# Performance work log

Hardware: AMD Instinct MI355X
Metric: run time of the kernel (lower is better)

The kernel has to match this reference:

```python
import jax, jax.numpy as jnp
import numpy as np

D_MODEL, N_LAYERS, D_INNER, D_STATE, D_CONV, DT_RANK, NUM_CLASSES = 256, 4, 512, 16, 4, 16, 10
B, L = 8, 1024


def setup_inputs() -> dict:
    key = jax.random.key(0)
    ks = jax.random.split(key, 16)
    s = 0.02
    inp = {}
    inp['x'] = jax.random.normal(ks[0], (B, L, 1), jnp.float32)
    inp['input_w'] = jax.random.normal(ks[1], (D_MODEL, 1), jnp.float32) * s
    inp['input_b'] = jnp.zeros((D_MODEL,), jnp.float32)
    inp['ln_w'] = jnp.ones((N_LAYERS, D_MODEL), jnp.float32)
    inp['ln_b'] = jnp.zeros((N_LAYERS, D_MODEL), jnp.float32)
    inp['in_proj_w'] = jax.random.normal(ks[2], (N_LAYERS, 2 * D_INNER, D_MODEL), jnp.float32) * s
    inp['in_proj_b'] = jnp.zeros((N_LAYERS, 2 * D_INNER), jnp.float32)
    inp['conv_w'] = jax.random.normal(ks[3], (N_LAYERS, D_INNER, 1, D_CONV), jnp.float32) * 0.2
    inp['conv_b'] = jnp.zeros((N_LAYERS, D_INNER), jnp.float32)
    inp['x_proj_w'] = jax.random.normal(ks[4], (N_LAYERS, DT_RANK + 2 * D_STATE, D_INNER), jnp.float32) * s
    inp['dt_proj_w'] = jax.random.normal(ks[5], (N_LAYERS, D_INNER, DT_RANK), jnp.float32) * s
    inp['dt_proj_b'] = jax.random.normal(ks[6], (N_LAYERS, D_INNER), jnp.float32) * 0.1 - 4.0  # small softplus(dt)
    # canonical S4D-real init: A = [1..d_state] repeated over d_inner
    A = jnp.tile(jnp.arange(1, D_STATE + 1, dtype=jnp.float32)[None, :], (D_INNER, 1))
    inp['A_log'] = jnp.tile(jnp.log(A)[None], (N_LAYERS, 1, 1))
    inp['D'] = jnp.ones((N_LAYERS, D_INNER), jnp.float32)
    inp['out_proj_w'] = jax.random.normal(ks[7], (N_LAYERS, D_MODEL, D_INNER), jnp.float32) * s
    inp['out_proj_b'] = jnp.zeros((N_LAYERS, D_MODEL), jnp.float32)
    inp['norm_w'] = jnp.ones((D_MODEL,), jnp.float32)
    inp['norm_b'] = jnp.zeros((D_MODEL,), jnp.float32)
    inp['cls_w'] = jax.random.normal(ks[8], (NUM_CLASSES, D_MODEL), jnp.float32) * s
    inp['cls_b'] = jnp.zeros((NUM_CLASSES,), jnp.float32)
    return inp


def _layernorm(x, w, b, eps=1e-5):
    mu = jnp.mean(x, axis=-1, keepdims=True)
    var = jnp.mean(jnp.square(x - mu), axis=-1, keepdims=True)
    return (x - mu) * jax.lax.rsqrt(var + eps) * w + b


def _causal_depthwise_conv(u, w, b):
    # u: (B, L, D_inner), w: (D_inner, 1, K), causal padding K-1
    out = jax.lax.conv_general_dilated(
        u.transpose(0, 2, 1), w, window_strides=(1,), padding=[(D_CONV - 1, 0)],
        feature_group_count=D_INNER, dimension_numbers=('NCH', 'OIH', 'NCH'))
    return out.transpose(0, 2, 1) + b


def _selective_scan(u, delta, A, Bm, Cm, Dp):
    # u, delta: (B,L,Din); Bm, Cm: (B,L,N); A: (Din,N); Dp: (Din,)
    def step(h, inp):
        d_t, B_t, C_t, u_t = inp                       # (B,Din),(B,N),(B,N),(B,Din)
        dA = jnp.exp(d_t[:, :, None] * A)              # (B,Din,N)
        dBu = d_t[:, :, None] * B_t[:, None, :] * u_t[:, :, None]
        h = dA * h + dBu
        y = jnp.einsum('bdn,bn->bd', h, C_t)
        return h, y
    h0 = jnp.zeros((u.shape[0], D_INNER, D_STATE), u.dtype)
    xs = (delta.transpose(1, 0, 2), Bm.transpose(1, 0, 2), Cm.transpose(1, 0, 2), u.transpose(1, 0, 2))
    _, ys = jax.lax.scan(step, h0, xs)                 # ys: (L,B,Din)
    return ys.transpose(1, 0, 2) + u * Dp


def _mamba_layer(x, ln_w, ln_b, ipw, ipb, cw, cb, xpw, dtw, dtb, A_log, Dp, opw, opb):
    h = _layernorm(x, ln_w, ln_b)
    xz = jnp.einsum('bld,ed->ble', h, ipw) + ipb       # (B,L,2*Din)
    u, res = jnp.split(xz, 2, axis=-1)
    u = jax.nn.silu(_causal_depthwise_conv(u, cw, cb))
    x_dbl = jnp.einsum('bld,ed->ble', u, xpw)          # (B,L,dt_rank+2N)
    dt, Bm, Cm = jnp.split(x_dbl, [DT_RANK, DT_RANK + D_STATE], axis=-1)
    delta = jax.nn.softplus(jnp.einsum('blr,dr->bld', dt, dtw) + dtb)
    A = -jnp.exp(A_log)
    y = _selective_scan(u, delta, A, Bm, Cm, Dp)
    y = y * jax.nn.silu(res)
    return x + jnp.einsum('ble,de->bld', y, opw) + opb


def reference(x, input_w, input_b, ln_w, ln_b, in_proj_w, in_proj_b, conv_w, conv_b,
              x_proj_w, dt_proj_w, dt_proj_b, A_log, D, out_proj_w, out_proj_b,
              norm_w, norm_b, cls_w, cls_b):
    h = jnp.einsum('blc,dc->bld', x, input_w) + input_b   # (B,L,D_MODEL)
    for i in range(N_LAYERS):
        h = _mamba_layer(h, ln_w[i], ln_b[i], in_proj_w[i], in_proj_b[i], conv_w[i], conv_b[i],
                         x_proj_w[i], dt_proj_w[i], dt_proj_b[i], A_log[i], D[i],
                         out_proj_w[i], out_proj_b[i])
    h = _layernorm(h, norm_w, norm_b)
    pooled = jnp.mean(h, axis=1)                          # (B, D_MODEL)
    return jnp.einsum('bd,cd->bc', pooled, cls_w) + cls_b
```

## Files before the change

kernel.cpp:

```cpp
#include <hip/hip_runtime.h>
#include <hip/hip_bf16.h>
#include <math.h>

#define DM 256
#define NL 4
#define DI 512
#define DS 16
#define DC 4
#define DR 16
#define NC 10
#define NB 8
#define LL 1024
#define MR (NB*LL)
#define NCHUNK 64
#define CLEN 16

typedef __attribute__((ext_vector_type(4))) float f32x4;
typedef __attribute__((ext_vector_type(8))) short short8;

__device__ __forceinline__ float silu_f(float x) {
    return x * (1.0f / (1.0f + __expf(-x)));
}
__device__ __forceinline__ float bf2f(ushort v) {
    union { unsigned u; float f; } c; c.u = ((unsigned)v) << 16; return c.f;
}
__device__ __forceinline__ ushort f2bf(float f) {
    union { float f; unsigned u; } c; c.f = f;
    unsigned lsb = (c.u >> 16) & 1;
    return (ushort)((c.u + 0x7fffu + lsb) >> 16);
}
__device__ __forceinline__ void g2lds16(const void* g, void* l) {
    __builtin_amdgcn_global_load_lds((const __attribute__((address_space(1))) void*)g,
                                     (__attribute__((address_space(3))) void*)l, 16, 0, 0);
}

#define IPW_N (NL*2*DI*DM)
#define XPW_N (NL*64*DI)
#define OPW_N (NL*DM*DI)
__global__ __launch_bounds__(256) void convert_weights_kernel(
        const float* __restrict__ ipw, const float* __restrict__ xpw,
        const float* __restrict__ opw,
        ushort* __restrict__ ipw_b, ushort* __restrict__ xpw_b, ushort* __restrict__ opw_b) {
    int t = blockIdx.x * 256 + threadIdx.x;
    if (t < IPW_N) { ipw_b[t] = f2bf(ipw[t]); return; }
    t -= IPW_N;
    if (t < XPW_N) {
        int l = t >> 15, r = (t >> 9) & 63, k = t & 511;
        xpw_b[t] = (r < 48) ? f2bf(xpw[((size_t)l * 48 + r) * DI + k]) : (ushort)0;
        return;
    }
    t -= XPW_N;
    if (t < OPW_N) opw_b[t] = f2bf(opw[t]);
}

__global__ void input_proj_kernel(const float* __restrict__ x, const float* __restrict__ w,
                                  const float* __restrict__ b, float* __restrict__ h) {
    int t = blockIdx.x * 256 + threadIdx.x;
    if (t >= MR * DM) return;
    int d = t & (DM - 1);
    int m = t >> 8;
    h[t] = x[m] * w[d] + b[d];
}

__global__ __launch_bounds__(256) void layernorm_bf16_kernel(const float* __restrict__ in,
        const float* __restrict__ w, const float* __restrict__ b, ushort* __restrict__ out) {
    int row = blockIdx.x, t = threadIdx.x;
    float v = in[row * DM + t];
    float s = v, q = v * v;
#pragma unroll
    for (int o = 32; o >= 1; o >>= 1) { s += __shfl_xor(s, o); q += __shfl_xor(q, o); }
    __shared__ float red[8];
    int wid = t >> 6;
    if ((t & 63) == 0) { red[wid] = s; red[4 + wid] = q; }
    __syncthreads();
    s = red[0] + red[1] + red[2] + red[3];
    q = red[4] + red[5] + red[6] + red[7];
    float mu = s * (1.0f / DM);
    float var = q * (1.0f / DM) - mu * mu;
    float rs = rsqrtf(var + 1e-5f);
    out[row * DM + t] = f2bf((v - mu) * rs * w[t] + b[t]);
}

template<int BM, int BN, int WM, int WN, int MODE>
__global__ __launch_bounds__(256) void mfma_gemm_kernel(
        const ushort* __restrict__ A, int lda,
        const ushort* __restrict__ W,
        const float* __restrict__ bias,
        ushort* __restrict__ Cb, float* __restrict__ Cf, int ldc, int K) {
    constexpr int FM = BM / WM / 16;
    constexpr int FN = BN / WN / 16;
    __shared__ __align__(16) char smem[(BM + BN) * 128];
    const int tid = threadIdx.x;
    const int l = tid & 63, w = tid >> 6;
    const int wr = w / WN, wc = w % WN;
    const int bm = blockIdx.x * BM, bn = blockIdx.y * BN;
    const int ldw = K;

    f32x4 acc[FM][FN] = {};

    for (int k0 = 0; k0 < K; k0 += 64) {
#pragma unroll
        for (int i = 0; i < (BM * 128 / 16) / 256; i++) {
            int lin = (i * 256 + tid) * 16;
            int q = lin ^ (((lin >> 7) & 7) << 4);
            g2lds16(A + (size_t)(bm + (q >> 7)) * lda + k0 + ((q & 127) >> 1), smem + lin);
        }
#pragma unroll
        for (int i = 0; i < (BN * 128 / 16) / 256; i++) {
            int lin = (i * 256 + tid) * 16;
            int q = lin ^ (((lin >> 7) & 7) << 4);
            g2lds16(W + (size_t)(bn + (q >> 7)) * ldw + k0 + ((q & 127) >> 1),
                    smem + BM * 128 + lin);
        }
        __syncthreads();
        const int rl = l & 15;
        const int kb0 = ((l >> 4) << 3) * 2;
#pragma unroll
        for (int kk = 0; kk < 2; kk++) {
            short8 af[FM], bfr[FN];
#pragma unroll
            for (int m = 0; m < FM; m++) {
                int off = (wr * (BM / WM) + m * 16 + rl) * 128 + kk * 64 + kb0;
                off ^= ((off >> 7) & 7) << 4;
                af[m] = *(const short8*)(smem + off);
            }
#pragma unroll
            for (int n = 0; n < FN; n++) {
                int off = (wc * (BN / WN) + n * 16 + rl) * 128 + kk * 64 + kb0;
                off ^= ((off >> 7) & 7) << 4;
                bfr[n] = *(const short8*)(smem + BM * 128 + off);
            }
#pragma unroll
            for (int m = 0; m < FM; m++)
#pragma unroll
                for (int n = 0; n < FN; n++)
                    acc[m][n] = __builtin_amdgcn_mfma_f32_16x16x32_bf16(
                        af[m], bfr[n], acc[m][n], 0, 0, 0);
        }
        __syncthreads();
    }

    const int row0 = bm + wr * (BM / WM) + ((l >> 4) << 2);
    const int col0 = bn + wc * (BN / WN) + (l & 15);
#pragma unroll
    for (int m = 0; m < FM; m++) {
#pragma unroll
        for (int n = 0; n < FN; n++) {
            int col = col0 + n * 16;
            float bv = (MODE == 1) ? 0.f : bias[col];
#pragma unroll
            for (int r = 0; r < 4; r++) {
                size_t idx = (size_t)(row0 + m * 16 + r) * ldc + col;
                float v = acc[m][n][r];
                if (MODE == 0) Cb[idx] = f2bf(v + bv);
                else if (MODE == 1) Cf[idx] = v;
                else Cf[idx] += v + bv;
            }
        }
    }
}

__global__ __launch_bounds__(256) void conv_silu_kernel(const ushort* __restrict__ xz,
        const float* __restrict__ cw, const float* __restrict__ cb, ushort* __restrict__ u) {
    int t = blockIdx.x * 256 + threadIdx.x;
    int d8 = (t & 63) << 3;
    int m = t >> 6;
    int l = m & (LL - 1);
    const short8 zr = {0, 0, 0, 0, 0, 0, 0, 0};
    const size_t base = (size_t)m * 1024 + d8;
    short8 r3 = *(const short8*)(xz + base);
    short8 r2 = (l >= 1) ? *(const short8*)(xz + base - 1024) : zr;
    short8 r1 = (l >= 2) ? *(const short8*)(xz + base - 2048) : zr;
    short8 r0 = (l >= 3) ? *(const short8*)(xz + base - 3072) : zr;
    short8 o;
#pragma unroll
    for (int j = 0; j < 8; j++) {
        int d = d8 + j;
        float4 w4 = *reinterpret_cast<const float4*>(&cw[d * 4]);
        float a = cb[d] + w4.w * bf2f((ushort)r3[j]);
        a += w4.z * bf2f((ushort)r2[j]);
        a += w4.y * bf2f((ushort)r1[j]);
        a += w4.x * bf2f((ushort)r0[j]);
        o[j] = (short)f2bf(silu_f(a));
    }
    *(short8*)(u + (size_t)m * DI + d8) = o;
}

__global__ __launch_bounds__(256) void dtproj_kernel(const float* __restrict__ x_dbl,
        const float* __restrict__ dtw, const float* __restrict__ dtb, float* __restrict__ delta) {
    int m0 = (blockIdx.x >> 1) * 32;
    int d = ((blockIdx.x & 1) << 8) + threadIdx.x;
    __shared__ float dts[32][17];
    {
        int i0 = threadIdx.x * 2;
        int r = i0 >> 4, k = i0 & 15;
        float2 v = *reinterpret_cast<const float2*>(&x_dbl[(size_t)(m0 + r) * 64 + k]);
        dts[r][k] = v.x; dts[r][k + 1] = v.y;
    }
    __syncthreads();
    float wreg[16];
#pragma unroll
    for (int q = 0; q < 4; q++) {
        float4 w4 = *reinterpret_cast<const float4*>(&dtw[d * DR + q * 4]);
        wreg[q*4] = w4.x; wreg[q*4+1] = w4.y; wreg[q*4+2] = w4.z; wreg[q*4+3] = w4.w;
    }
    float bv = dtb[d];
    for (int r = 0; r < 32; r++) {
        float acc = bv;
#pragma unroll
        for (int k = 0; k < DR; k++) acc += wreg[k] * dts[r][k];
        float sp = (acc > 20.0f) ? acc : __logf(1.0f + __expf(acc));
        delta[(size_t)(m0 + r) * DI + d] = sp;
    }
}

__global__ __launch_bounds__(256, 4) void scan_phase1_kernel(
        const ushort* __restrict__ u, const float* __restrict__ delta,
        const float* __restrict__ x_dbl, const float* __restrict__ A_log,
        float* __restrict__ sdv, float* __restrict__ Sbuf) {
    int gid = blockIdx.x * 256 + threadIdx.x;
    int d = gid & (DI - 1);
    int c = (gid >> 9) & (NCHUNK - 1);
    int b = gid >> 15;
    float Aval[DS], h[DS];
#pragma unroll
    for (int q = 0; q < 4; q++) {
        float4 a4 = *reinterpret_cast<const float4*>(&A_log[d * DS + q * 4]);
        Aval[q*4+0] = -__expf(a4.x); Aval[q*4+1] = -__expf(a4.y);
        Aval[q*4+2] = -__expf(a4.z); Aval[q*4+3] = -__expf(a4.w);
    }
#pragma unroll
    for (int n = 0; n < DS; n++) h[n] = 0.f;
    int m0 = b * LL + c * CLEN;
    const float* dp = delta + (size_t)m0 * DI + d;
    const ushort* up = u + (size_t)m0 * DI + d;
    const float* xb = x_dbl + (size_t)m0 * 64 + 16;
    float sd = 0.f;
    float dv = dp[0];
    float uv = bf2f(up[0]);
    float Bv[DS];
#pragma unroll
    for (int q = 0; q < 4; q++) {
        float4 b4 = *reinterpret_cast<const float4*>(xb + q * 4);
        Bv[q*4] = b4.x; Bv[q*4+1] = b4.y; Bv[q*4+2] = b4.z; Bv[q*4+3] = b4.w;
    }
    for (int t = 0; t < CLEN; t++) {
        float dvn = 0.f, uvn = 0.f, Bn[DS];
#pragma unroll
        for (int n = 0; n < DS; n++) Bn[n] = 0.f;
        if (t + 1 < CLEN) {
            dvn = dp[(size_t)(t + 1) * DI];
            uvn = bf2f(up[(size_t)(t + 1) * DI]);
            const float* xbn = xb + (size_t)(t + 1) * 64;
#pragma unroll
            for (int q = 0; q < 4; q++) {
                float4 b4 = *reinterpret_cast<const float4*>(xbn + q * 4);
                Bn[q*4] = b4.x; Bn[q*4+1] = b4.y; Bn[q*4+2] = b4.z; Bn[q*4+3] = b4.w;
            }
        }
        sd += dv;
        float du = dv * uv;
#pragma unroll
        for (int n = 0; n < DS; n++) {
            float dA = __expf(dv * Aval[n]);
            h[n] = dA * h[n] + du * Bv[n];
        }
        dv = dvn; uv = uvn;
#pragma unroll
        for (int n = 0; n < DS; n++) Bv[n] = Bn[n];
    }
    size_t base = ((size_t)((b * NCHUNK + c) * DI + d)) * DS;
#pragma unroll
    for (int q = 0; q < 4; q++)
        *reinterpret_cast<float4*>(&Sbuf[base + q * 4]) =
            make_float4(h[q*4], h[q*4+1], h[q*4+2], h[q*4+3]);
    sdv[(b * NCHUNK + c) * DI + d] = sd;
}

__global__ __launch_bounds__(256) void scan_phase2_kernel(
        const float* __restrict__ sdv, const float* __restrict__ A_log,
        float* __restrict__ Sbuf) {
    int gid = blockIdx.x * 256 + threadIdx.x;
    int dn = gid & (DI * DS - 1);
    int b = gid >> 13;
    int n = dn & 15, d = dn >> 4;
    float Aval = -__expf(A_log[d * DS + n]);
    size_t idx0 = (size_t)b * NCHUNK * DI * DS + dn;
    const size_t stride = (size_t)DI * DS;
    int sb0 = b * NCHUNK * DI + d;
    float h = 0.f;
    float Sc = Sbuf[idx0];
    float sd = sdv[sb0];
    for (int c = 0; c < NCHUNK; c++) {
        size_t idx = idx0 + (size_t)c * stride;
        float Sn = 0.f, sdn = 0.f;
        if (c + 1 < NCHUNK) {
            Sn = Sbuf[idx + stride];
            sdn = sdv[sb0 + (c + 1) * DI];
        }
        float Pc = __expf(Aval * sd);
        Sbuf[idx] = h;
        h = Pc * h + Sc;
        Sc = Sn; sd = sdn;
    }
}

__global__ __launch_bounds__(256, 4) void scan_phase3_kernel(
        const ushort* __restrict__ u, const float* __restrict__ delta,
        const float* __restrict__ x_dbl, const float* __restrict__ A_log,
        const float* __restrict__ Dp, const float* __restrict__ Sbuf,
        const ushort* __restrict__ xz, ushort* __restrict__ y) {
    int gid = blockIdx.x * 256 + threadIdx.x;
    int d = gid & (DI - 1);
    int c = (gid >> 9) & (NCHUNK - 1);
    int b = gid >> 15;
    float Aval[DS], h[DS];
#pragma unroll
    for (int q = 0; q < 4; q++) {
        float4 a4 = *reinterpret_cast<const float4*>(&A_log[d * DS + q * 4]);
        Aval[q*4+0] = -__expf(a4.x); Aval[q*4+1] = -__expf(a4.y);
        Aval[q*4+2] = -__expf(a4.z); Aval[q*4+3] = -__expf(a4.w);
    }
    size_t base = ((size_t)((b * NCHUNK + c) * DI + d)) * DS;
#pragma unroll
    for (int q = 0; q < 4; q++) {
        float4 h4 = *reinterpret_cast<const float4*>(&Sbuf[base + q * 4]);
        h[q*4] = h4.x; h[q*4+1] = h4.y; h[q*4+2] = h4.z; h[q*4+3] = h4.w;
    }
    float Dval = Dp[d];
    int m0 = b * LL + c * CLEN;
    const float* dp = delta + (size_t)m0 * DI + d;
    const ushort* up = u + (size_t)m0 * DI + d;
    const float* xb = x_dbl + (size_t)m0 * 64 + 16;
    const ushort* rp = xz + (size_t)m0 * 1024 + 512 + d;
    ushort* yp = y + (size_t)m0 * DI + d;
    float dv = dp[0];
    float uv = bf2f(up[0]);
    float rv = bf2f(rp[0]);
    float Bv[DS], Cv[DS];
#pragma unroll
    for (int q = 0; q < 4; q++) {
        float4 b4 = *reinterpret_cast<const float4*>(xb + q * 4);
        float4 c4 = *reinterpret_cast<const float4*>(xb + 16 + q * 4);
        Bv[q*4] = b4.x; Bv[q*4+1] = b4.y; Bv[q*4+2] = b4.z; Bv[q*4+3] = b4.w;
        Cv[q*4] = c4.x; Cv[q*4+1] = c4.y; Cv[q*4+2] = c4.z; Cv[q*4+3] = c4.w;
    }
    for (int t = 0; t < CLEN; t++) {
        float dvn = 0.f, uvn = 0.f, rvn = 0.f, Bn[DS], Cn[DS];
#pragma unroll
        for (int n = 0; n < DS; n++) { Bn[n] = 0.f; Cn[n] = 0.f; }
        if (t + 1 < CLEN) {
            dvn = dp[(size_t)(t + 1) * DI];
            uvn = bf2f(up[(size_t)(t + 1) * DI]);
            rvn = bf2f(rp[(size_t)(t + 1) * 1024]);
            const float* xbn = xb + (size_t)(t + 1) * 64;
#pragma unroll
            for (int q = 0; q < 4; q++) {
                float4 b4 = *reinterpret_cast<const float4*>(xbn + q * 4);
                float4 c4 = *reinterpret_cast<const float4*>(xbn + 16 + q * 4);
                Bn[q*4] = b4.x; Bn[q*4+1] = b4.y; Bn[q*4+2] = b4.z; Bn[q*4+3] = b4.w;
                Cn[q*4] = c4.x; Cn[q*4+1] = c4.y; Cn[q*4+2] = c4.z; Cn[q*4+3] = c4.w;
            }
        }
        float du = dv * uv;
        float acc = Dval * uv;
#pragma unroll
        for (int n = 0; n < DS; n++) {
            float dA = __expf(dv * Aval[n]);
            h[n] = dA * h[n] + du * Bv[n];
            acc += h[n] * Cv[n];
        }
        yp[(size_t)t * DI] = f2bf(acc * silu_f(rv));
        dv = dvn; uv = uvn; rv = rvn;
#pragma unroll
        for (int n = 0; n < DS; n++) { Bv[n] = Bn[n]; Cv[n] = Cn[n]; }
    }
}

__global__ __launch_bounds__(256) void pool_partial_kernel(const ushort* __restrict__ ln,
                                                           float* __restrict__ partial) {
    int bs = blockIdx.x;
    int b = bs >> 3, sl = bs & 7;
    int t = threadIdx.x;
    int l0 = sl * 128;
    float s = 0.f;
    for (int l = 0; l < 128; l++) s += bf2f(ln[(size_t)(b * LL + l0 + l) * DM + t]);
    partial[(bs << 8) + t] = s;
}

__global__ void cls_kernel(const float* __restrict__ partial, const float* __restrict__ cw,
                           const float* __restrict__ cb, float* __restrict__ out) {
    int t = threadIdx.x;
    if (t >= NB * NC) return;
    int b = t / NC, c = t % NC;
    float s = 0.f;
    for (int k = 0; k < DM; k++) {
        float p = 0.f;
#pragma unroll
        for (int sl = 0; sl < 8; sl++) p += partial[((b * 8 + sl) << 8) + k];
        s += p * cw[c * DM + k];
    }
    out[t] = cb[c] + s * (1.0f / LL);
}

extern "C" void kernel_launch(void* const* d_in, const int* in_sizes, int n_in,
                              void* d_out, int out_size, void* d_ws, size_t ws_size,
                              hipStream_t stream) {
    const float* x       = (const float*)d_in[0];
    const float* input_w = (const float*)d_in[1];
    const float* input_b = (const float*)d_in[2];
    const float* ln_w    = (const float*)d_in[3];
    const float* ln_b    = (const float*)d_in[4];
    const float* ipw     = (const float*)d_in[5];
    const float* ipb     = (const float*)d_in[6];
    const float* cw      = (const float*)d_in[7];
    const float* cb      = (const float*)d_in[8];
    const float* xpw     = (const float*)d_in[9];
    const float* dtw     = (const float*)d_in[10];
    const float* dtb     = (const float*)d_in[11];
    const float* A_log   = (const float*)d_in[12];
    const float* Dp      = (const float*)d_in[13];
    const float* opw     = (const float*)d_in[14];
    const float* opb     = (const float*)d_in[15];
    const float* norm_w  = (const float*)d_in[16];
    const float* norm_b  = (const float*)d_in[17];
    const float* cls_w   = (const float*)d_in[18];
    const float* cls_b   = (const float*)d_in[19];
    float* out = (float*)d_out;
    float* ws = (float*)d_ws;

    float*  hres   = ws;
    ushort* xz     = (ushort*)(hres + (size_t)MR * DM);
    ushort* ub     = xz + (size_t)MR * 1024;
    float*  delta  = (float*)(ub + (size_t)MR * DI);
    float*  x_dbl  = delta + (size_t)MR * DI;
    float*  sdvb   = x_dbl + (size_t)MR * 64;
    float*  Sbuf   = sdvb + (size_t)NB * NCHUNK * DI;
    float*  partial= Sbuf + (size_t)NB * NCHUNK * DI * DS;
    ushort* ygate  = (ushort*)(partial + 64 * 256);
    ushort* hln    = ygate + (size_t)MR * DI;
    ushort* ipw_b  = hln + (size_t)MR * DM;
    ushort* xpw_b  = ipw_b + IPW_N;
    ushort* opw_b  = xpw_b + XPW_N;

    convert_weights_kernel<<<(IPW_N + XPW_N + OPW_N) / 256, 256, 0, stream>>>(
        ipw, xpw, opw, ipw_b, xpw_b, opw_b);
    input_proj_kernel<<<MR * DM / 256, 256, 0, stream>>>(x, input_w, input_b, hres);

    for (int i = 0; i < NL; i++) {
        layernorm_bf16_kernel<<<MR, 256, 0, stream>>>(hres, ln_w + i * DM, ln_b + i * DM, hln);
        mfma_gemm_kernel<128, 128, 2, 2, 0><<<dim3(MR / 128, 1024 / 128), 256, 0, stream>>>(
            hln, DM, ipw_b + (size_t)i * 2 * DI * DM, ipb + (size_t)i * 2 * DI,
            xz, nullptr, 1024, DM);
        conv_silu_kernel<<<MR * DI / 8 / 256, 256, 0, stream>>>(xz, cw + i * DI * DC, cb + i * DI, ub);
        mfma_gemm_kernel<64, 64, 4, 1, 1><<<dim3(MR / 64, 1), 256, 0, stream>>>(
            ub, DI, xpw_b + (size_t)i * 64 * DI, nullptr, nullptr, x_dbl, 64, DI);
        dtproj_kernel<<<(MR / 32) * 2, 256, 0, stream>>>(
            x_dbl, dtw + i * DI * DR, dtb + i * DI, delta);
        scan_phase1_kernel<<<NB * NCHUNK * DI / 256, 256, 0, stream>>>(
            ub, delta, x_dbl, A_log + i * DI * DS, sdvb, Sbuf);
        scan_phase2_kernel<<<NB * DI * DS / 256, 256, 0, stream>>>(
            sdvb, A_log + i * DI * DS, Sbuf);
        scan_phase3_kernel<<<NB * NCHUNK * DI / 256, 256, 0, stream>>>(
            ub, delta, x_dbl, A_log + i * DI * DS, Dp + i * DI, Sbuf, xz, ygate);
        mfma_gemm_kernel<64, 128, 2, 2, 2><<<dim3(MR / 64, DM / 128), 256, 0, stream>>>(
            ygate, DI, opw_b + (size_t)i * DM * DI, opb + (size_t)i * DM,
            nullptr, hres, DM, DI);
    }

    layernorm_bf16_kernel<<<MR, 256, 0, stream>>>(hres, norm_w, norm_b, hln);
    pool_partial_kernel<<<64, 256, 0, stream>>>(hln, partial);
    cls_kernel<<<1, 128, 0, stream>>>(partial, cls_w, cls_b, out);
}
```

Measured before the change: 513.9 us.

## Fuse dt projection and softplus into both selective scan phases

Removes the separate dtproj kernel and its fp32 delta buffer (MR x DI floats written once and read twice per layer). Both scan phase 1 and phase 3 now recompute delta per timestep from the 16 dt columns of x_dbl, using per-channel dt weights held in registers. B and C are read directly from x_dbl each step instead of being prefetched into register arrays, and phase 3 splits its state reduction into four partial sums. The trade is extra ALU work (a 16-term dot product plus softplus, done twice) and possibly more register pressure, in exchange for less HBM traffic and one fewer launch per layer.

```diff
diff --git a/kernel.cpp b/kernel.cpp
--- a/kernel.cpp
+++ b/kernel.cpp
@@ -186,88 +186,53 @@
     *(short8*)(u + (size_t)m * DI + d8) = o;
 }
 
-__global__ __launch_bounds__(256) void dtproj_kernel(const float* __restrict__ x_dbl,
-        const float* __restrict__ dtw, const float* __restrict__ dtb, float* __restrict__ delta) {
-    int m0 = (blockIdx.x >> 1) * 32;
-    int d = ((blockIdx.x & 1) << 8) + threadIdx.x;
-    __shared__ float dts[32][17];
-    {
-        int i0 = threadIdx.x * 2;
-        int r = i0 >> 4, k = i0 & 15;
-        float2 v = *reinterpret_cast<const float2*>(&x_dbl[(size_t)(m0 + r) * 64 + k]);
-        dts[r][k] = v.x; dts[r][k + 1] = v.y;
-    }
-    __syncthreads();
-    float wreg[16];
-#pragma unroll
-    for (int q = 0; q < 4; q++) {
-        float4 w4 = *reinterpret_cast<const float4*>(&dtw[d * DR + q * 4]);
-        wreg[q*4] = w4.x; wreg[q*4+1] = w4.y; wreg[q*4+2] = w4.z; wreg[q*4+3] = w4.w;
-    }
-    float bv = dtb[d];
-    for (int r = 0; r < 32; r++) {
-        float acc = bv;
-#pragma unroll
-        for (int k = 0; k < DR; k++) acc += wreg[k] * dts[r][k];
-        float sp = (acc > 20.0f) ? acc : __logf(1.0f + __expf(acc));
-        delta[(size_t)(m0 + r) * DI + d] = sp;
-    }
-}
-
 __global__ __launch_bounds__(256, 4) void scan_phase1_kernel(
-        const ushort* __restrict__ u, const float* __restrict__ delta,
-        const float* __restrict__ x_dbl, const float* __restrict__ A_log,
+        const ushort* __restrict__ u, const float* __restrict__ x_dbl,
+        const float* __restrict__ A_log,
+        const float* __restrict__ dtw, const float* __restrict__ dtb,
         float* __restrict__ sdv, float* __restrict__ Sbuf) {
     int gid = blockIdx.x * 256 + threadIdx.x;
     int d = gid & (DI - 1);
     int c = (gid >> 9) & (NCHUNK - 1);
     int b = gid >> 15;
-    float Aval[DS], h[DS];
+    float Aval[DS], h[DS], wreg[DR];
 #pragma unroll
     for (int q = 0; q < 4; q++) {
         float4 a4 = *reinterpret_cast<const float4*>(&A_log[d * DS + q * 4]);
         Aval[q*4+0] = -__expf(a4.x); Aval[q*4+1] = -__expf(a4.y);
         Aval[q*4+2] = -__expf(a4.z); Aval[q*4+3] = -__expf(a4.w);
-    }
+        float4 w4 = *reinterpret_cast<const float4*>(&dtw[d * DR + q * 4]);
+        wreg[q*4] = w4.x; wreg[q*4+1] = w4.y; wreg[q*4+2] = w4.z; wreg[q*4+3] = w4.w;
+    }
+    float dbv = dtb[d];
 #pragma unroll
     for (int n = 0; n < DS; n++) h[n] = 0.f;
     int m0 = b * LL + c * CLEN;
-    const float* dp = delta + (size_t)m0 * DI + d;
+    const float* xb = x_dbl + (size_t)m0 * 64;
     const ushort* up = u + (size_t)m0 * DI + d;
-    const float* xb = x_dbl + (size_t)m0 * 64 + 16;
     float sd = 0.f;
-    float dv = dp[0];
     float uv = bf2f(up[0]);
-    float Bv[DS];
-#pragma unroll
-    for (int q = 0; q < 4; q++) {
-        float4 b4 = *reinterpret_cast<const float4*>(xb + q * 4);
-        Bv[q*4] = b4.x; Bv[q*4+1] = b4.y; Bv[q*4+2] = b4.z; Bv[q*4+3] = b4.w;
-    }
     for (int t = 0; t < CLEN; t++) {
-        float dvn = 0.f, uvn = 0.f, Bn[DS];
-#pragma unroll
-        for (int n = 0; n < DS; n++) Bn[n] = 0.f;
-        if (t + 1 < CLEN) {
-            dvn = dp[(size_t)(t + 1) * DI];
-            uvn = bf2f(up[(size_t)(t + 1) * DI]);
-            const float* xbn = xb + (size_t)(t + 1) * 64;
-#pragma unroll
-            for (int q = 0; q < 4; q++) {
-                float4 b4 = *reinterpret_cast<const float4*>(xbn + q * 4);
-                Bn[q*4] = b4.x; Bn[q*4+1] = b4.y; Bn[q*4+2] = b4.z; Bn[q*4+3] = b4.w;
-            }
-        }
+        float uvn = (t + 1 < CLEN) ? bf2f(up[(size_t)(t + 1) * DI]) : 0.f;
+        const float* xr = xb + (size_t)t * 64;
+        float p0 = dbv, p1 = 0.f, p2 = 0.f, p3 = 0.f;
+#pragma unroll
+        for (int k = 0; k < 4; k++) {
+            p0 += wreg[k] * xr[k];
+            p1 += wreg[4 + k] * xr[4 + k];
+            p2 += wreg[8 + k] * xr[8 + k];
+            p3 += wreg[12 + k] * xr[12 + k];
+        }
+        float z = (p0 + p1) + (p2 + p3);
+        float dv = (z > 20.0f) ? z : __logf(1.0f + __expf(z));
         sd += dv;
         float du = dv * uv;
 #pragma unroll
         for (int n = 0; n < DS; n++) {
             float dA = __expf(dv * Aval[n]);
-            h[n] = dA * h[n] + du * Bv[n];
-        }
-        dv = dvn; uv = uvn;
-#pragma unroll
-        for (int n = 0; n < DS; n++) Bv[n] = Bn[n];
+            h[n] = dA * h[n] + du * xr[16 + n];
+        }
+        uv = uvn;
     }
     size_t base = ((size_t)((b * NCHUNK + c) * DI + d)) * DS;
 #pragma unroll
@@ -306,21 +271,25 @@
 }
 
 __global__ __launch_bounds__(256, 4) void scan_phase3_kernel(
-        const ushort* __restrict__ u, const float* __restrict__ delta,
-        const float* __restrict__ x_dbl, const float* __restrict__ A_log,
+        const ushort* __restrict__ u, const float* __restrict__ x_dbl,
+        const float* __restrict__ A_log,
+        const float* __restrict__ dtw, const float* __restrict__ dtb,
         const float* __restrict__ Dp, const float* __restrict__ Sbuf,
         const ushort* __restrict__ xz, ushort* __restrict__ y) {
     int gid = blockIdx.x * 256 + threadIdx.x;
     int d = gid & (DI - 1);
     int c = (gid >> 9) & (NCHUNK - 1);
     int b = gid >> 15;
-    float Aval[DS], h[DS];
+    float Aval[DS], h[DS], wreg[DR];
 #pragma unroll
     for (int q = 0; q < 4; q++) {
         float4 a4 = *reinterpret_cast<const float4*>(&A_log[d * DS + q * 4]);
         Aval[q*4+0] = -__expf(a4.x); Aval[q*4+1] = -__expf(a4.y);
         Aval[q*4+2] = -__expf(a4.z); Aval[q*4+3] = -__expf(a4.w);
-    }
+        float4 w4 = *reinterpret_cast<const float4*>(&dtw[d * DR + q * 4]);
+        wreg[q*4] = w4.x; wreg[q*4+1] = w4.y; wreg[q*4+2] = w4.z; wreg[q*4+3] = w4.w;
+    }
+    float dbv = dtb[d];
     size_t base = ((size_t)((b * NCHUNK + c) * DI + d)) * DS;
 #pragma unroll
     for (int q = 0; q < 4; q++) {
@@ -329,51 +298,61 @@
     }
     float Dval = Dp[d];
     int m0 = b * LL + c * CLEN;
-    const float* dp = delta + (size_t)m0 * DI + d;
+    const float* xb = x_dbl + (size_t)m0 * 64;
     const ushort* up = u + (size_t)m0 * DI + d;
-    const float* xb = x_dbl + (size_t)m0 * 64 + 16;
     const ushort* rp = xz + (size_t)m0 * 1024 + 512 + d;
     ushort* yp = y + (size_t)m0 * DI + d;
-    float dv = dp[0];
     float uv = bf2f(up[0]);
     float rv = bf2f(rp[0]);
-    float Bv[DS], Cv[DS];
-#pragma unroll
-    for (int q = 0; q < 4; q++) {
-        float4 b4 = *reinterpret_cast<const float4*>(xb + q * 4);
-        float4 c4 = *reinterpret_cast<const float4*>(xb + 16 + q * 4);
-        Bv[q*4] = b4.x; Bv[q*4+1] = b4.y; Bv[q*4+2] = b4.z; Bv[q*4+3] = b4.w;
-        Cv[q*4] = c4.x; Cv[q*4+1] = c4.y; Cv[q*4+2] = c4.z; Cv[q*4+3] = c4.w;
-    }
     for (int t = 0; t < CLEN; t++) {
-        float dvn = 0.f, uvn = 0.f, rvn = 0.f, Bn[DS], Cn[DS];
-#pragma unroll
-        for (int n = 0; n < DS; n++) { Bn[n] = 0.f; Cn[n] = 0.f; }
+        float uvn = 0.f, rvn = 0.f;
         if (t + 1 < CLEN) {
-            dvn = dp[(size_t)(t + 1) * DI];
             uvn = bf2f(up[(size_t)(t + 1) * DI]);
             rvn = bf2f(rp[(size_t)(t + 1) * 1024]);
-            const float* xbn = xb + (size_t)(t + 1) * 64;
-#pragma unroll
-            for (int q = 0; q < 4; q++) {
-                float4 b4 = *reinterpret_cast<const float4*>(xbn + q * 4);
-                float4 c4 = *reinterpret_cast<const float4*>(xbn + 16 + q * 4);
-                Bn[q*4] = b4.x; Bn[q*4+1] = b4.y; Bn[q*4+2] = b4.z; Bn[q*4+3] = b4.w;
-                Cn[q*4] = c4.x; Cn[q*4+1] = c4.y; Cn[q*4+2] = c4.z; Cn[q*4+3] = c4.w;
-            }
-        }
+        }
+        const float* xr = xb + (size_t)t * 64;
+        float p0 = dbv, p1 = 0.f, p2 = 0.f, p3 = 0.f;
+#pragma unroll
+        for (int k = 0; k < 4; k++) {
+            p0 += wreg[k] * xr[k];
+            p1 += wreg[4 + k] * xr[4 + k];
+            p2 += wreg[8 + k] * xr[8 + k];
+            p3 += wreg[12 + k] * xr[12 + k];
+        }
+        float z = (p0 + p1) + (p2 + p3);
+        float dv = (z > 20.0f) ? z : __logf(1.0f + __expf(z));
         float du = dv * uv;
-        float acc = Dval * uv;
-#pragma unroll
-        for (int n = 0; n < DS; n++) {
-            float dA = __expf(dv * Aval[n]);
-            h[n] = dA * h[n] + du * Bv[n];
-            acc += h[n] * Cv[n];
-        }
+        float a0 = 0.f, a1 = 0.f, a2 = 0.f, a3 = 0.f;
+#pragma unroll
+        for (int j = 0; j < 4; j++) {
+            {
+                int n = j;
+                float dA = __expf(dv * Aval[n]);
+                h[n] = dA * h[n] + du * xr[16 + n];
+                a0 += h[n] * xr[32 + n];
+            }
+            {
+                int n = 4 + j;
+                float dA = __expf(dv * Aval[n]);
+                h[n] = dA * h[n] + du * xr[16 + n];
+                a1 += h[n] * xr[32 + n];
+            }
+            {
+                int n = 8 + j;
+                float dA = __expf(dv * Aval[n]);
+                h[n] = dA * h[n] + du * xr[16 + n];
+                a2 += h[n] * xr[32 + n];
+            }
+            {
+                int n = 12 + j;
+                float dA = __expf(dv * Aval[n]);
+                h[n] = dA * h[n] + du * xr[16 + n];
+                a3 += h[n] * xr[32 + n];
+            }
+        }
+        float acc = ((a0 + a1) + (a2 + a3)) + Dval * uv;
         yp[(size_t)t * DI] = f2bf(acc * silu_f(rv));
-        dv = dvn; uv = uvn; rv = rvn;
-#pragma unroll
-        for (int n = 0; n < DS; n++) { Bv[n] = Bn[n]; Cv[n] = Cn[n]; }
+        uv = uvn; rv = rvn;
     }
 }
 
@@ -432,8 +411,7 @@
     float*  hres   = ws;
     ushort* xz     = (ushort*)(hres + (size_t)MR * DM);
     ushort* ub     = xz + (size_t)MR * 1024;
-    float*  delta  = (float*)(ub + (size_t)MR * DI);
-    float*  x_dbl  = delta + (size_t)MR * DI;
+    float*  x_dbl  = (float*)(ub + (size_t)MR * DI);
     float*  sdvb   = x_dbl + (size_t)MR * 64;
     float*  Sbuf   = sdvb + (size_t)NB * NCHUNK * DI;
     float*  partial= Sbuf + (size_t)NB * NCHUNK * DI * DS;
@@ -455,14 +433,13 @@
         conv_silu_kernel<<<MR * DI / 8 / 256, 256, 0, stream>>>(xz, cw + i * DI * DC, cb + i * DI, ub);
         mfma_gemm_kernel<64, 64, 4, 1, 1><<<dim3(MR / 64, 1), 256, 0, stream>>>(
             ub, DI, xpw_b + (size_t)i * 64 * DI, nullptr, nullptr, x_dbl, 64, DI);
-        dtproj_kernel<<<(MR / 32) * 2, 256, 0, stream>>>(
-            x_dbl, dtw + i * DI * DR, dtb + i * DI, delta);
         scan_phase1_kernel<<<NB * NCHUNK * DI / 256, 256, 0, stream>>>(
-            ub, delta, x_dbl, A_log + i * DI * DS, sdvb, Sbuf);
+            ub, x_dbl, A_log + i * DI * DS, dtw + i * DI * DR, dtb + i * DI, sdvb, Sbuf);
         scan_phase2_kernel<<<NB * DI * DS / 256, 256, 0, stream>>>(
             sdvb, A_log + i * DI * DS, Sbuf);
         scan_phase3_kernel<<<NB * NCHUNK * DI / 256, 256, 0, stream>>>(
-            ub, delta, x_dbl, A_log + i * DI * DS, Dp + i * DI, Sbuf, xz, ygate);
+            ub, x_dbl, A_log + i * DI * DS, dtw + i * DI * DR, dtb + i * DI,
+            Dp + i * DI, Sbuf, xz, ygate);
         mfma_gemm_kernel<64, 128, 2, 2, 2><<<dim3(MR / 64, DM / 128), 256, 0, stream>>>(
             ygate, DI, opw_b + (size_t)i * DM * DI, opb + (size_t)i * DM,
             nullptr, hres, DM, DI);
```

Measured after the change: 558.1 us. 8.6% more time.
